# Kernel optimization log

Measured on AMD Instinct MI355X. Metric: run time of the kernel, lower is better.

## Reference

```python
import jax, jax.numpy as jnp
import numpy as np

N = 16384      # total ligand atoms
E = 65536      # edges
B = 256        # graphs / batch
MAXN = 64      # atoms per graph (max_nodes for to_dense_batch)
FIN = 64       # num_node_features
HID = 256      # hidden_channels
GH = 2         # gat heads
LP = 1024      # protein length
NH = 4         # cross-attention heads
HD = HID // NH
VOCAB = 22


def setup_inputs() -> dict:
    key = jax.random.key(0)
    ks = jax.random.split(key, 48)
    f = jnp.float32
    def nrm(k, shape, s=0.05):
        return jax.random.normal(k, shape, f) * s
    inp = {}
    inp["x"] = jax.random.normal(ks[0], (N, FIN), f)
    inp["edge_index"] = jax.random.randint(ks[1], (2, E), 0, N)
    inp["batch"] = jnp.arange(N) // MAXN  # sorted, 64 atoms per graph
    inp["protein_seq"] = jax.random.randint(ks[2], (B, LP), 0, VOCAB)
    # GAT layer 1 (FIN -> HID, GH heads, concat=False)
    inp["w1"] = nrm(ks[3], (FIN, GH * HID)); inp["as1"] = nrm(ks[4], (GH, HID)); inp["ad1"] = nrm(ks[5], (GH, HID)); inp["b1"] = jnp.zeros((HID,), f)
    inp["w2"] = nrm(ks[6], (HID, GH * HID)); inp["as2"] = nrm(ks[7], (GH, HID)); inp["ad2"] = nrm(ks[8], (GH, HID)); inp["b2"] = jnp.zeros((HID,), f)
    inp["w3"] = nrm(ks[9], (HID, GH * HID)); inp["as3"] = nrm(ks[10], (GH, HID)); inp["ad3"] = nrm(ks[11], (GH, HID)); inp["b3"] = jnp.zeros((HID,), f)
    # protein embedding + conv1d (OIH layout)
    inp["emb"] = nrm(ks[12], (VOCAB, HID), 0.1)
    inp["conv_w"] = nrm(ks[13], (HID, HID, 3)); inp["conv_b"] = jnp.zeros((HID,), f)
    # cross-attention MHA
    inp["wq"] = nrm(ks[14], (HID, HID)); inp["bq"] = jnp.zeros((HID,), f)
    inp["wk"] = nrm(ks[15], (HID, HID)); inp["bk"] = jnp.zeros((HID,), f)
    inp["wv"] = nrm(ks[16], (HID, HID)); inp["bv"] = jnp.zeros((HID,), f)
    inp["wo"] = nrm(ks[17], (HID, HID)); inp["bo"] = jnp.zeros((HID,), f)
    inp["ln1_g"] = jnp.ones((HID,), f); inp["ln1_b"] = jnp.zeros((HID,), f)
    inp["ffw1"] = nrm(ks[18], (HID, 4 * HID)); inp["ffb1"] = jnp.zeros((4 * HID,), f)
    inp["ffw2"] = nrm(ks[19], (4 * HID, HID)); inp["ffb2"] = jnp.zeros((HID,), f)
    inp["ln2_g"] = jnp.ones((HID,), f); inp["ln2_b"] = jnp.zeros((HID,), f)
    inp["fc1_w"] = nrm(ks[20], (HID, HID)); inp["fc1_b"] = jnp.zeros((HID,), f)
    inp["fc2_w"] = nrm(ks[21], (HID, 1)); inp["fc2_b"] = jnp.zeros((1,), f)
    return inp


def _gat(x, edge_index, W, a_src, a_dst, bias):
    # PyG GATConv, concat=False (mean over heads), add_self_loops=True
    n = x.shape[0]
    h = (x @ W).reshape(n, GH, HID)                      # [N,GH,C]
    loop = jnp.arange(n)
    src = jnp.concatenate([edge_index[0], loop])
    dst = jnp.concatenate([edge_index[1], loop])
    a_s = jnp.einsum('nhc,hc->nh', h, a_src)             # [N,GH]
    a_d = jnp.einsum('nhc,hc->nh', h, a_dst)
    e = jax.nn.leaky_relu(a_s[src] + a_d[dst], 0.2)      # [E+N,GH]
    emax = jax.ops.segment_max(e, dst, num_segments=n)   # each node has a self-loop
    ex = jnp.exp(e - emax[dst])
    den = jax.ops.segment_sum(ex, dst, num_segments=n)
    alpha = ex / den[dst]                                # [E+N,GH]
    msg = h[src] * alpha[:, :, None]
    out = jax.ops.segment_sum(msg, dst, num_segments=n)  # [N,GH,C]
    return out.mean(axis=1) + bias


def _to_dense_batch(x, batch):
    # batch is sorted node->graph ids; counts per graph <= MAXN
    ones = jnp.ones((x.shape[0],), jnp.int32)
    counts = jax.ops.segment_sum(ones, batch, num_segments=B)
    starts = jnp.cumsum(counts) - counts
    pos = jnp.arange(x.shape[0]) - starts[batch]
    dense = jnp.zeros((B, MAXN, x.shape[1]), x.dtype).at[batch, pos].set(x)
    mask = jnp.zeros((B, MAXN), bool).at[batch, pos].set(True)
    return dense, mask


def _layernorm(x, g, b, eps=1e-5):
    mu = x.mean(-1, keepdims=True)
    var = ((x - mu) ** 2).mean(-1, keepdims=True)
    return (x - mu) * jax.lax.rsqrt(var + eps) * g + b


def reference(x, edge_index, batch, protein_seq,
              w1, as1, ad1, b1, w2, as2, ad2, b2, w3, as3, ad3, b3,
              emb, conv_w, conv_b,
              wq, bq, wk, bk, wv, bv, wo, bo,
              ln1_g, ln1_b, ffw1, ffb1, ffw2, ffb2, ln2_g, ln2_b,
              fc1_w, fc1_b, fc2_w, fc2_b):
    # --- ligand GNN (eval mode: dropout = identity) ---
    h = jax.nn.elu(_gat(x, edge_index, w1, as1, ad1, b1))
    h = jax.nn.elu(_gat(h, edge_index, w2, as2, ad2, b2))
    h = jax.nn.elu(_gat(h, edge_index, w3, as3, ad3, b3))
    lig, lig_mask = _to_dense_batch(h, batch)            # [B,MAXN,HID], [B,MAXN]
    # --- protein branch ---
    p = emb[protein_seq]                                 # [B,LP,HID]
    p = p.transpose(0, 2, 1)                             # [B,HID,LP]
    p = jax.lax.conv_general_dilated(p, conv_w, (1,), [(1, 1)],
                                     dimension_numbers=('NCH', 'OIH', 'NCH'))
    p = jax.nn.relu(p + conv_b[None, :, None]).transpose(0, 2, 1)  # [B,LP,HID]
    kpm = protein_seq == 0                               # key padding mask
    # --- cross attention (query=ligand, key/value=protein) ---
    q = (lig @ wq + bq).reshape(B, MAXN, NH, HD)
    k = (p @ wk + bk).reshape(B, LP, NH, HD)
    v = (p @ wv + bv).reshape(B, LP, NH, HD)
    scores = jnp.einsum('bqhd,bkhd->bhqk', q, k) / np.sqrt(HD).astype(np.float32)
    scores = jnp.where(kpm[:, None, None, :], jnp.float32(-1e9), scores)
    attn = jax.nn.softmax(scores, axis=-1)               # [B,NH,MAXN,LP]
    ctx = jnp.einsum('bhqk,bkhd->bqhd', attn, v).reshape(B, MAXN, HID)
    attn_out = ctx @ wo + bo
    y = _layernorm(lig + attn_out, ln1_g, ln1_b)
    ff = jax.nn.gelu(y @ ffw1 + ffb1, approximate=False) @ ffw2 + ffb2
    y = _layernorm(y + ff, ln2_g, ln2_b)
    # --- masked mean pool ---
    m = lig_mask[:, :, None].astype(y.dtype)
    pooled = (y * m).sum(axis=1) / (m.sum(axis=1) + 1e-6)
    out = jax.nn.relu(pooled @ fc1_w + fc1_b)
    return out @ fc2_w + fc2_b                           # [B,1]
```

## Files before the change

kernel.cpp:

```cpp
#include <hip/hip_runtime.h>
#include <hip/hip_bf16.h>
#include <cstdint>
#include <cstddef>

#define NAT 16384
#define NED 65536
#define BGR 256
#define FIN 64
#define HID 256
#define LPN 1024
#define HD 64
#define NTRIP 11638
#define NTAB  11648

typedef __bf16 bf16x8 __attribute__((ext_vector_type(8)));
typedef float floatx4 __attribute__((ext_vector_type(4)));

__device__ __forceinline__ void gl2lds16(const void* g, void* l)
{
    __builtin_amdgcn_global_load_lds(
        (const __attribute__((address_space(1))) unsigned int*)g,
        (__attribute__((address_space(3))) unsigned int*)l, 16, 0, 0);
}

template<int ACT, int OUTBF16, int BIASROW, int HSPLIT, int NCOL>
__global__ __launch_bounds__(512) void gemm_mfma(const __bf16* __restrict__ A,
    const __bf16* __restrict__ Bt, const float* __restrict__ bias,
    void* __restrict__ Cout, int M, int Nn, int K, float escale)
{
    constexpr int NJ = NCOL / 32;
    __shared__ __bf16 As[2][128][32];
    __shared__ __bf16 Bs[2][NCOL][32];
    const int t = threadIdx.x;
    const int m0 = blockIdx.y * 128, n0 = blockIdx.x * NCOL;
    const int w = t >> 6, lane = t & 63;
    const int wm = (w & 3) * 32, wn = (w >> 2) * (NCOL / 2);
    const int quad = lane >> 4, l16 = lane & 15;
    const int r0 = t >> 2, s0 = t & 3, g0 = (s0 ^ (r0 & 3)) * 8;
    const int fso = (quad ^ (l16 & 3)) * 8;
    floatx4 acc[2][NJ] = {};
    for (int k0 = 0; k0 < K; k0 += 64) {
        gl2lds16(A + (size_t)(m0 + r0) * K + k0 + g0,       &As[0][r0][s0 * 8]);
        gl2lds16(A + (size_t)(m0 + r0) * K + k0 + 32 + g0,  &As[1][r0][s0 * 8]);
        if (NCOL == 128 || t < 256) {
            gl2lds16(Bt + (size_t)(n0 + r0) * K + k0 + g0,      &Bs[0][r0][s0 * 8]);
            gl2lds16(Bt + (size_t)(n0 + r0) * K + k0 + 32 + g0, &Bs[1][r0][s0 * 8]);
        }
        __syncthreads();
#pragma unroll
        for (int c = 0; c < 2; c++) {
            bf16x8 af[2], bfr[NJ];
#pragma unroll
            for (int mi = 0; mi < 2; mi++) af[mi]  = *(const bf16x8*)&As[c][wm + mi * 16 + l16][fso];
#pragma unroll
            for (int nj = 0; nj < NJ; nj++) bfr[nj] = *(const bf16x8*)&Bs[c][wn + nj * 16 + l16][fso];
#pragma unroll
            for (int mi = 0; mi < 2; mi++)
#pragma unroll
                for (int nj = 0; nj < NJ; nj++)
                    acc[mi][nj] = __builtin_amdgcn_mfma_f32_16x16x32_bf16(af[mi], bfr[nj], acc[mi][nj], 0, 0, 0);
        }
        __syncthreads();
    }
#pragma unroll
    for (int mi = 0; mi < 2; mi++)
#pragma unroll
        for (int nj = 0; nj < NJ; nj++) {
            int col = n0 + wn + nj * 16 + l16;
#pragma unroll
            for (int r = 0; r < 4; r++) {
                int row = m0 + wm + mi * 16 + quad * 4 + r;
                float bval = bias ? (BIASROW ? bias[row] : bias[col]) : 0.f;
                float v = (acc[mi][nj][r] + bval) * escale;
                if (ACT == 1) v = fmaxf(v, 0.f);
                if (ACT == 2) v = 0.5f * v * (1.f + erff(v * 0.70710678118654752f));
                if (HSPLIT)      ((__bf16*)Cout)[((size_t)(col >> 6) * M + row) * 64 + (col & 63)] = (__bf16)v;
                else if (OUTBF16) ((__bf16*)Cout)[(size_t)row * Nn + col] = (__bf16)v;
                else              ((float*)Cout)[(size_t)row * Nn + col] = v;
            }
        }
}

__global__ __launch_bounds__(512) void kvtab_k(const __bf16* __restrict__ A,
    const __bf16* __restrict__ wkT, const __bf16* __restrict__ wvT,
    const float* __restrict__ bk, const float* __restrict__ bv,
    __bf16* __restrict__ Ktab, __bf16* __restrict__ Vtab)
{
    __shared__ __bf16 As[2][128][32];
    __shared__ __bf16 Bs[2][128][32];
    const int t = threadIdx.x;
    const int z = blockIdx.x >> 1;
    const int m0 = blockIdx.y * 128, n0 = (blockIdx.x & 1) * 128;
    const __bf16* Bt = z ? wvT : wkT;
    const float* bias = z ? bv : bk;
    __bf16* Cout = z ? Vtab : Ktab;
    const int w = t >> 6, lane = t & 63;
    const int wm = (w & 3) * 32, wn = (w >> 2) * 64;
    const int quad = lane >> 4, l16 = lane & 15;
    const int r0 = t >> 2, s0 = t & 3, g0 = (s0 ^ (r0 & 3)) * 8;
    const int fso = (quad ^ (l16 & 3)) * 8;
    floatx4 acc[2][4] = {};
    for (int k0 = 0; k0 < 256; k0 += 64) {
        gl2lds16(A + (size_t)(m0 + r0) * 256 + k0 + g0,       &As[0][r0][s0 * 8]);
        gl2lds16(A + (size_t)(m0 + r0) * 256 + k0 + 32 + g0,  &As[1][r0][s0 * 8]);
        gl2lds16(Bt + (size_t)(n0 + r0) * 256 + k0 + g0,      &Bs[0][r0][s0 * 8]);
        gl2lds16(Bt + (size_t)(n0 + r0) * 256 + k0 + 32 + g0, &Bs[1][r0][s0 * 8]);
        __syncthreads();
#pragma unroll
        for (int c = 0; c < 2; c++) {
            bf16x8 af[2], bfr[4];
#pragma unroll
            for (int mi = 0; mi < 2; mi++) af[mi]  = *(const bf16x8*)&As[c][wm + mi * 16 + l16][fso];
#pragma unroll
            for (int nj = 0; nj < 4; nj++) bfr[nj] = *(const bf16x8*)&Bs[c][wn + nj * 16 + l16][fso];
#pragma unroll
            for (int mi = 0; mi < 2; mi++)
#pragma unroll
                for (int nj = 0; nj < 4; nj++)
                    acc[mi][nj] = __builtin_amdgcn_mfma_f32_16x16x32_bf16(af[mi], bfr[nj], acc[mi][nj], 0, 0, 0);
        }
        __syncthreads();
    }
#pragma unroll
    for (int mi = 0; mi < 2; mi++)
#pragma unroll
        for (int nj = 0; nj < 4; nj++) {
            int col = n0 + wn + nj * 16 + l16;
#pragma unroll
            for (int r = 0; r < 4; r++) {
                int row = m0 + wm + mi * 16 + quad * 4 + r;
                float v = acc[mi][nj][r] + bias[col];
                Cout[((size_t)(col >> 6) * NTAB + row) * 64 + (col & 63)] = (__bf16)v;
            }
        }
}

__global__ __launch_bounds__(512) void gemm_gat(const __bf16* __restrict__ A,
    const __bf16* __restrict__ Bt, const float* __restrict__ as_f,
    const float* __restrict__ ad_f, __bf16* __restrict__ Hg,
    float* __restrict__ part, int K)
{
    __shared__ __bf16 As[2][128][32];
    __shared__ __bf16 Bs[2][128][32];
    const int t = threadIdx.x;
    const int m0 = blockIdx.y * 128, n0 = blockIdx.x * 128;
    const int w = t >> 6, lane = t & 63;
    const int wm = (w & 3) * 32, wn = (w >> 2) * 64;
    const int quad = lane >> 4, l16 = lane & 15;
    const int r0 = t >> 2, s0 = t & 3, g0 = (s0 ^ (r0 & 3)) * 8;
    const int fso = (quad ^ (l16 & 3)) * 8;
    floatx4 acc[2][4] = {};
    for (int k0 = 0; k0 < K; k0 += 64) {
        gl2lds16(A + (size_t)(m0 + r0) * K + k0 + g0,       &As[0][r0][s0 * 8]);
        gl2lds16(A + (size_t)(m0 + r0) * K + k0 + 32 + g0,  &As[1][r0][s0 * 8]);
        gl2lds16(Bt + (size_t)(n0 + r0) * K + k0 + g0,      &Bs[0][r0][s0 * 8]);
        gl2lds16(Bt + (size_t)(n0 + r0) * K + k0 + 32 + g0, &Bs[1][r0][s0 * 8]);
        __syncthreads();
#pragma unroll
        for (int c = 0; c < 2; c++) {
            bf16x8 af[2], bfr[4];
#pragma unroll
            for (int mi = 0; mi < 2; mi++) af[mi]  = *(const bf16x8*)&As[c][wm + mi * 16 + l16][fso];
#pragma unroll
            for (int nj = 0; nj < 4; nj++) bfr[nj] = *(const bf16x8*)&Bs[c][wn + nj * 16 + l16][fso];
#pragma unroll
            for (int mi = 0; mi < 2; mi++)
#pragma unroll
                for (int nj = 0; nj < 4; nj++)
                    acc[mi][nj] = __builtin_amdgcn_mfma_f32_16x16x32_bf16(af[mi], bfr[nj], acc[mi][nj], 0, 0, 0);
        }
        __syncthreads();
    }
    const int slot = blockIdx.x * 2 + (w >> 2);
#pragma unroll
    for (int mi = 0; mi < 2; mi++) {
#pragma unroll
        for (int r = 0; r < 4; r++) {
            float ps = 0.f, pd = 0.f;
#pragma unroll
            for (int nj = 0; nj < 4; nj++) {
                int col = n0 + wn + nj * 16 + l16;
                float v = acc[mi][nj][r];
                ps += v * as_f[col];
                pd += v * ad_f[col];
            }
#pragma unroll
            for (int off = 1; off < 16; off <<= 1) {
                ps += __shfl_xor(ps, off, 64);
                pd += __shfl_xor(pd, off, 64);
            }
            if (l16 == 0) {
                int row = m0 + wm + mi * 16 + quad * 4 + r;
                part[(size_t)(slot * 2 + 0) * NAT + row] = ps;
                part[(size_t)(slot * 2 + 1) * NAT + row] = pd;
            }
        }
    }
#pragma unroll
    for (int mi = 0; mi < 2; mi++)
#pragma unroll
        for (int nj = 0; nj < 4; nj++) {
            int col = n0 + wn + nj * 16 + l16;
#pragma unroll
            for (int r = 0; r < 4; r++) {
                int row = m0 + wm + mi * 16 + quad * 4 + r;
                Hg[(size_t)row * 512 + col] = (__bf16)acc[mi][nj][r];
            }
        }
}

__global__ void fold_k(const float* __restrict__ part, float* __restrict__ a_s,
                       float* __restrict__ a_d)
{
    int n = blockIdx.x * 256 + threadIdx.x;
    float s0 = 0.f, d0 = 0.f, s1 = 0.f, d1 = 0.f;
#pragma unroll
    for (int sl = 0; sl < 4; sl++) {
        s0 += part[(size_t)(sl * 2 + 0) * NAT + n];
        d0 += part[(size_t)(sl * 2 + 1) * NAT + n];
        s1 += part[(size_t)((sl + 4) * 2 + 0) * NAT + n];
        d1 += part[(size_t)((sl + 4) * 2 + 1) * NAT + n];
    }
    a_s[n * 2 + 0] = s0; a_s[n * 2 + 1] = s1;
    a_d[n * 2 + 0] = d0; a_d[n * 2 + 1] = d1;
}

__global__ __launch_bounds__(256) void tap_k(const float* __restrict__ emb,
    const float* __restrict__ cw, float* __restrict__ tap)
{
    const int dlv = blockIdx.x >> 2, part = blockIdx.x & 3;
    const int dl = dlv / 22, v = dlv % 22;
    const int n = threadIdx.x;
    const float* er = emb + v * 256 + part * 64;
    const float* wr = cw + (size_t)n * 768 + part * 192 + dl;
    float s = 0.f;
    for (int k = 0; k < 64; k += 4) {
        s += er[k + 0] * wr[k * 3 + 0];
        s += er[k + 1] * wr[k * 3 + 3];
        s += er[k + 2] * wr[k * 3 + 6];
        s += er[k + 3] * wr[k * 3 + 9];
    }
    atomicAdd(&tap[(size_t)dlv * 256 + n], s);
}

__global__ __launch_bounds__(256) void ptab_k(const float* __restrict__ tap,
    const float* __restrict__ bias, __bf16* __restrict__ P)
{
    const int t = threadIdx.x;
    const int row = blockIdx.x * 8 + (t >> 5);
    const int c = (t & 31) * 8;
    __bf16 o[8];
    if (row < NTRIP) {
        const int a = row / 506, rem = row - a * 506;
        const int t1 = rem / 23, c2 = rem - t1 * 23;
        float acc[8];
#pragma unroll
        for (int j = 0; j < 8; j++) acc[j] = bias[c + j];
        if (a > 0) {
            const float* r = tap + (size_t)(0 * 22 + (a - 1)) * 256 + c;
#pragma unroll
            for (int j = 0; j < 8; j++) acc[j] += r[j];
        }
        {
            const float* r = tap + (size_t)(1 * 22 + t1) * 256 + c;
#pragma unroll
            for (int j = 0; j < 8; j++) acc[j] += r[j];
        }
        if (c2 > 0) {
            const float* r = tap + (size_t)(2 * 22 + (c2 - 1)) * 256 + c;
#pragma unroll
            for (int j = 0; j < 8; j++) acc[j] += r[j];
        }
#pragma unroll
        for (int j = 0; j < 8; j++) o[j] = (__bf16)fmaxf(acc[j], 0.f);
    } else {
#pragma unroll
        for (int j = 0; j < 8; j++) o[j] = (__bf16)0.f;
    }
    *(uint4*)(P + (size_t)row * 256 + c) = *(uint4*)o;
}

__global__ void tid_k(const int* __restrict__ seq, unsigned short* __restrict__ tid)
{
    int i = blockIdx.x * 256 + threadIdx.x;
    int b = i >> 10, l = i & 1023;
    const int* sr = seq + b * LPN;
    int t0 = (l > 0) ? sr[l - 1] : -1;
    int t1 = sr[l];
    int t2 = (l < LPN - 1) ? sr[l + 1] : -1;
    int v = (t0 + 1) * 506 + t1 * 23 + (t2 + 1);
    tid[i] = (unsigned short)(v | (t1 == 0 ? 0x8000 : 0));
}

struct Segs {
    const float* src[12];
    __bf16* dst[12];
    int kdim[12];
    int ndim[12];
    int mode[12];
    int start[13];
};

__global__ void cvtall_k(Segs S, int total)
{
    int i = blockIdx.x * 256 + threadIdx.x;
    if (i >= total) return;
    int s = 0;
    while (i >= S.start[s + 1]) s++;
    int j = i - S.start[s];
    if (S.mode[s] == 0) {
        S.dst[s][j] = (__bf16)S.src[s][j];
    } else {
        int K = S.kdim[s], N = S.ndim[s];
        int n = j / K, k = j - n * K;
        S.dst[s][j] = (__bf16)S.src[s][(size_t)k * N + n];
    }
}

__global__ void deg_k(const int* __restrict__ ei, int* __restrict__ deg)
{
    int e = blockIdx.x * 256 + threadIdx.x;
    if (e < NED) atomicAdd(&deg[ei[NED + e]], 1);
}

__global__ __launch_bounds__(256) void scan_k(const int* __restrict__ deg, int* __restrict__ rowptr)
{
    __shared__ int part[256];
    int t = threadIdx.x;
    int base = t * 64;
    int s = 0;
#pragma unroll
    for (int i = 0; i < 64; i++) s += deg[base + i];
    part[t] = s;
    __syncthreads();
    for (int off = 1; off < 256; off <<= 1) {
        int v = (t >= off) ? part[t - off] : 0;
        __syncthreads();
        part[t] += v;
        __syncthreads();
    }
    int run = t ? part[t - 1] : 0;
    for (int i = 0; i < 64; i++) { rowptr[base + i] = run; run += deg[base + i]; }
    if (t == 255) rowptr[16384] = run;
}

__global__ void scat_k(const int* __restrict__ ei, int* __restrict__ fill,
                       const int* __restrict__ rowptr, int* __restrict__ csrc,
                       int* __restrict__ cdst)
{
    int e = blockIdx.x * 256 + threadIdx.x;
    if (e >= NED) return;
    int d = ei[NED + e];
    int pos = rowptr[d] + atomicAdd(&fill[d], 1);
    csrc[pos] = ei[e];
    cdst[pos] = d;
}

__global__ void erec_k(const int* __restrict__ csrc, const int* __restrict__ cdst,
    const float* __restrict__ a_s, const float* __restrict__ a_d,
    float4* __restrict__ rec)
{
    int p = blockIdx.x * 256 + threadIdx.x;
    if (p >= NED) return;
    int s = csrc[p], d = cdst[p];
    float2 as2 = *(const float2*)(a_s + s * 2);
    float2 ad2 = *(const float2*)(a_d + d * 2);
    float e0 = as2.x + ad2.x; e0 = (e0 > 0.f) ? e0 : 0.2f * e0;
    float e1 = as2.y + ad2.y; e1 = (e1 > 0.f) ? e1 : 0.2f * e1;
    rec[p] = make_float4(e0, e1, __int_as_float(s), 0.f);
}

__global__ __launch_bounds__(256) void gat_agg(const int* __restrict__ rowptr,
    const float4* __restrict__ rec, const __bf16* __restrict__ hgb,
    const float* __restrict__ a_s, const float* __restrict__ a_d,
    const float* __restrict__ bias, float* __restrict__ out, __bf16* __restrict__ outb)
{
    const int wave = threadIdx.x >> 6, lane = threadIdx.x & 63;
    const int d = blockIdx.x * 4 + wave;
    const int beg = rowptr[d], end = rowptr[d + 1];
    float2 as2 = *(const float2*)(a_s + d * 2);
    float2 ad2 = *(const float2*)(a_d + d * 2);
    float e0 = as2.x + ad2.x; e0 = (e0 > 0.f) ? e0 : 0.2f * e0;
    float e1 = as2.y + ad2.y; e1 = (e1 > 0.f) ? e1 : 0.2f * e1;
    float m0 = e0, den0 = 1.f, m1 = e1, den1 = 1.f;
    for (int p = beg; p < end; p++) {
        float4 rc = rec[p];
        float nm0 = fmaxf(m0, rc.x);
        den0 = den0 * __expf(m0 - nm0) + __expf(rc.x - nm0);
        m0 = nm0;
        float nm1 = fmaxf(m1, rc.y);
        den1 = den1 * __expf(m1 - nm1) + __expf(rc.y - nm1);
        m1 = nm1;
    }
    const float inv0 = 1.f / den0, inv1 = 1.f / den1;
    const int ch = lane * 8;
    const int g = ch >> 8;
    const float mg = g ? m1 : m0, invg = g ? inv1 : inv0;
    float acc[8] = {};
    {
        float al = __expf((g ? e1 : e0) - mg) * invg;
        bf16x8 hv = *(const bf16x8*)(hgb + (size_t)d * 512 + ch);
#pragma unroll
        for (int j = 0; j < 8; j++) acc[j] += (float)hv[j] * al;
    }
    for (int p = beg; p < end; p++) {
        float4 rc = rec[p];
        float al = __expf((g ? rc.y : rc.x) - mg) * invg;
        int s = __float_as_int(rc.z);
        bf16x8 hv = *(const bf16x8*)(hgb + (size_t)s * 512 + ch);
#pragma unroll
        for (int j = 0; j < 8; j++) acc[j] += (float)hv[j] * al;
    }
    float other[8];
#pragma unroll
    for (int j = 0; j < 8; j++) other[j] = __shfl_xor(acc[j], 32, 64);
    if (lane < 32) {
#pragma unroll
        for (int j = 0; j < 8; j++) {
            float v = 0.5f * (acc[j] + other[j]) + bias[ch + j];
            v = (v > 0.f) ? v : expm1f(v);
            if (out) out[(size_t)d * 256 + ch + j] = v;
            outb[(size_t)d * 256 + ch + j] = (__bf16)v;
        }
    }
}

__global__ __launch_bounds__(256, 4) void attn6_k(const __bf16* __restrict__ Qb,
    const __bf16* __restrict__ Ktab, const __bf16* __restrict__ Vtab,
    const unsigned short* __restrict__ tid16, __bf16* __restrict__ O)
{
    __shared__ __bf16 Ks[2][4096];
    __shared__ __bf16 Vs[4096];
    __shared__ __bf16 Ps2[4][16][64];
    __shared__ float mask_f[1024];
    __shared__ unsigned short tids[1024];
    const int t = threadIdx.x;
    const int bid = blockIdx.x;
    const int h = (bid >> 1) & 3;
    const int b = ((bid >> 3) << 1) | (bid & 1);
    const int w = t >> 6, lane = t & 63;
    const int quad = lane >> 4, l16 = lane & 15;
    const int key = (l16 & 7) << 4;
    const __bf16* Kh = Ktab + (size_t)h * NTAB * 64;
    const __bf16* Vh = Vtab + (size_t)h * NTAB * 64;
    {
        const uint32_t* src = (const uint32_t*)(tid16 + (size_t)b * LPN);
        uint32_t v0 = src[t], v1 = src[t + 256];
        ((uint32_t*)tids)[t] = v0;
        ((uint32_t*)tids)[t + 256] = v1;
        mask_f[2 * t + 0] = (v0 & 0x8000u) ? -1e9f : 0.f;
        mask_f[2 * t + 1] = (v0 & 0x80000000u) ? -1e9f : 0.f;
        mask_f[2 * (t + 256) + 0] = (v1 & 0x8000u) ? -1e9f : 0.f;
        mask_f[2 * (t + 256) + 1] = (v1 & 0x80000000u) ? -1e9f : 0.f;
    }
    const __bf16* qrow = Qb + (size_t)(b * 64 + w * 16 + l16) * HID + h * HD;
    bf16x8 aq0 = *(const bf16x8*)(qrow + quad * 8);
    bf16x8 aq1 = *(const bf16x8*)(qrow + 32 + quad * 8);
    __syncthreads();

    auto stageK = [&](int kt, int bufb) {
#pragma unroll
        for (int it = 0; it < 2; it++) {
            const int s = it * 256 + t;
            const int pos = s >> 3;
            const int c = (s & 7) ^ (pos & 7);
            const int row = tids[kt * 64 + pos] & 0x7fff;
            gl2lds16(Kh + (size_t)row * 64 + c * 8,
                     &Ks[bufb][(it * 256 + w * 64) * 8]);
        }
    };
    auto loadV = [&](int kt, bf16x8* vrr) {
#pragma unroll
        for (int it = 0; it < 2; it++) {
            const int pos = w * 8 + (lane >> 3) + it * 32;
            const int row = tids[kt * 64 + pos] & 0x7fff;
            vrr[it] = *(const bf16x8*)(Vh + (size_t)row * 64 + (lane & 7) * 8);
        }
    };
    auto writeV = [&](const bf16x8* vrr) {
        const int p = lane >> 3, c = lane & 7;
#pragma unroll
        for (int it = 0; it < 2; it++) {
            const int pos = w * 8 + p + it * 32;
            const int cp = pos >> 3;
#pragma unroll
            for (int j = 0; j < 8; j++) {
                const int chl = c * 8 + j;
                Vs[chl * 64 + (((cp ^ c ^ j) & 7) << 3) + p] = vrr[it][j];
            }
        }
    };

    bf16x8 vr[2];
    stageK(0, 0);
    loadV(0, vr);
    writeV(vr);
    float m_run = -3e38f;
    float l_run = 0.f;
    floatx4 ctx[4] = {};
    __syncthreads();

    for (int kt = 0; kt < 16; kt++) {
        const int buf = kt & 1;
        const int kp0 = kt * 64;
        if (kt < 15) {
            stageK(kt + 1, buf ^ 1);
            loadV(kt + 1, vr);
        }
        const int ksl0 = (quad ^ (l16 & 7)) * 8;
        const int ksl1 = ((quad + 4) ^ (l16 & 7)) * 8;
        floatx4 s[4];
#pragma unroll
        for (int nj = 0; nj < 4; nj++) {
            const __bf16* kr = &Ks[buf][(nj * 16 + l16) * 64];
            bf16x8 k0 = *(const bf16x8*)&kr[ksl0];
            bf16x8 k1 = *(const bf16x8*)&kr[ksl1];
            floatx4 z = {0.f, 0.f, 0.f, 0.f};
            s[nj] = __builtin_amdgcn_mfma_f32_16x16x32_bf16(k0, aq0, z, 0, 0, 0);
            s[nj] = __builtin_amdgcn_mfma_f32_16x16x32_bf16(k1, aq1, s[nj], 0, 0, 0);
        }
#pragma unroll
        for (int nj = 0; nj < 4; nj++) {
            floatx4 m4 = *(const floatx4*)&mask_f[kp0 + nj * 16 + quad * 4];
#pragma unroll
            for (int r = 0; r < 4; r++) s[nj][r] += m4[r];
        }
        float mx = -3e38f;
#pragma unroll
        for (int nj = 0; nj < 4; nj++)
#pragma unroll
            for (int r = 0; r < 4; r++) mx = fmaxf(mx, s[nj][r]);
        mx = fmaxf(mx, __shfl_xor(mx, 16, 64));
        mx = fmaxf(mx, __shfl_xor(mx, 32, 64));
        const float mn = fmaxf(m_run, mx);
        const float alpha = __expf(m_run - mn);
        m_run = mn;
        float rs = 0.f;
#pragma unroll
        for (int nj = 0; nj < 4; nj++)
#pragma unroll
            for (int r = 0; r < 4; r++) {
                float p = __expf(s[nj][r] - mn);
                s[nj][r] = p;
                rs += p;
            }
        rs += __shfl_xor(rs, 16, 64);
        rs += __shfl_xor(rs, 32, 64);
        l_run = l_run * alpha + rs;
        float al[4];
#pragma unroll
        for (int r = 0; r < 4; r++) al[r] = __shfl(alpha, quad * 4 + r, 64);
        {
            char* rowp = (char*)&Ps2[w][l16][0];
#pragma unroll
            for (int nj = 0; nj < 4; nj++) {
                union { uint2 u2; unsigned short us[4]; } pk;
#pragma unroll
                for (int r = 0; r < 4; r++) {
                    __bf16 bv = (__bf16)s[nj][r];
                    pk.us[r] = *(unsigned short*)&bv;
                }
                *(uint2*)(rowp + ((nj * 32 + quad * 8) ^ key)) = pk.u2;
            }
        }
        bf16x8 pa0 = *(const bf16x8*)((char*)&Ps2[w][l16][0] + ((quad * 16) ^ key));
        bf16x8 pa1 = *(const bf16x8*)((char*)&Ps2[w][l16][0] + ((64 + quad * 16) ^ key));
#pragma unroll
        for (int dj = 0; dj < 4; dj++) {
#pragma unroll
            for (int r = 0; r < 4; r++) ctx[dj][r] *= al[r];
            const int chl = dj * 16 + l16;
            const int Xc = ((chl >> 3) ^ (chl & 7)) & 7;
            bf16x8 bv0 = *(const bf16x8*)&Vs[chl * 64 + (((quad ^ Xc) & 7) << 3)];
            bf16x8 bv1 = *(const bf16x8*)&Vs[chl * 64 + ((((quad + 4) ^ Xc) & 7) << 3)];
            ctx[dj] = __builtin_amdgcn_mfma_f32_16x16x32_bf16(pa0, bv0, ctx[dj], 0, 0, 0);
            ctx[dj] = __builtin_amdgcn_mfma_f32_16x16x32_bf16(pa1, bv1, ctx[dj], 0, 0, 0);
        }
        __syncthreads();
        if (kt < 15) writeV(vr);
        __syncthreads();
    }
    float ll[4];
#pragma unroll
    for (int r = 0; r < 4; r++) ll[r] = __shfl(l_run, quad * 4 + r, 64);
#pragma unroll
    for (int dj = 0; dj < 4; dj++)
#pragma unroll
        for (int r = 0; r < 4; r++) {
            int q = w * 16 + quad * 4 + r;
            O[((size_t)(b * 64 + q)) * 256 + h * HD + dj * 16 + l16] = (__bf16)(ctx[dj][r] / ll[r]);
        }
}

__device__ __forceinline__ float blockSum256(float v, float* red)
{
#pragma unroll
    for (int off = 32; off >= 1; off >>= 1) v += __shfl_down(v, off, 64);
    int wave = threadIdx.x >> 6, lane = threadIdx.x & 63;
    if (lane == 0) red[wave] = v;
    __syncthreads();
    float s = red[0] + red[1] + red[2] + red[3];
    __syncthreads();
    return s;
}

__global__ __launch_bounds__(256) void lnres_k(const float* __restrict__ A,
    const float* __restrict__ Bb, const float* __restrict__ g,
    const float* __restrict__ be, float* __restrict__ Y, __bf16* __restrict__ Yb)
{
    __shared__ float red[4];
    int r = blockIdx.x, t = threadIdx.x;
    float v = A[(size_t)r * 256 + t] + Bb[(size_t)r * 256 + t];
    float mean = blockSum256(v, red) * (1.f / 256.f);
    float d = v - mean;
    float var = blockSum256(d * d, red) * (1.f / 256.f);
    float o = d * rsqrtf(var + 1e-5f) * g[t] + be[t];
    Y[(size_t)r * 256 + t] = o;
    if (Yb) Yb[(size_t)r * 256 + t] = (__bf16)o;
}

__global__ __launch_bounds__(256) void head_k(const float* __restrict__ Y,
    const float* __restrict__ fc1w, const float* __restrict__ fc1b,
    const float* __restrict__ fc2w, const float* __restrict__ fc2b,
    float* __restrict__ out)
{
    __shared__ float pooled[256];
    __shared__ float h[256];
    __shared__ float red[4];
    int b = blockIdx.x, t = threadIdx.x;
    float s = 0.f;
#pragma unroll 8
    for (int q = 0; q < 64; q++) s += Y[(size_t)(b * 64 + q) * 256 + t];
    pooled[t] = s / (64.f + 1e-6f);
    __syncthreads();
    float a = 0.f;
    for (int k = 0; k < 256; k += 4) {
        a += pooled[k + 0] * fc1w[(k + 0) * 256 + t];
        a += pooled[k + 1] * fc1w[(k + 1) * 256 + t];
        a += pooled[k + 2] * fc1w[(k + 2) * 256 + t];
        a += pooled[k + 3] * fc1w[(k + 3) * 256 + t];
    }
    h[t] = fmaxf(a + fc1b[t], 0.f);
    __syncthreads();
    float p = h[t] * fc2w[t];
    p = blockSum256(p, red);
    if (t == 0) out[b] = p + fc2b[0];
}

extern "C" void kernel_launch(void* const* d_in, const int* in_sizes, int n_in,
                              void* d_out, int out_size, void* d_ws, size_t ws_size,
                              hipStream_t stream)
{
    const float* x     = (const float*)d_in[0];
    const int*   ei    = (const int*)d_in[1];
    const int*   pseq  = (const int*)d_in[3];
    const float* w1  = (const float*)d_in[4];
    const float* as1 = (const float*)d_in[5];
    const float* ad1 = (const float*)d_in[6];
    const float* b1  = (const float*)d_in[7];
    const float* w2  = (const float*)d_in[8];
    const float* as2 = (const float*)d_in[9];
    const float* ad2 = (const float*)d_in[10];
    const float* b2  = (const float*)d_in[11];
    const float* w3  = (const float*)d_in[12];
    const float* as3 = (const float*)d_in[13];
    const float* ad3 = (const float*)d_in[14];
    const float* b3  = (const float*)d_in[15];
    const float* emb    = (const float*)d_in[16];
    const float* conv_w = (const float*)d_in[17];
    const float* conv_b = (const float*)d_in[18];
    const float* wq = (const float*)d_in[19];
    const float* bq = (const float*)d_in[20];
    const float* wk = (const float*)d_in[21];
    const float* bk = (const float*)d_in[22];
    const float* wv = (const float*)d_in[23];
    const float* bv = (const float*)d_in[24];
    const float* wo = (const float*)d_in[25];
    const float* bo = (const float*)d_in[26];
    const float* ln1_g = (const float*)d_in[27];
    const float* ln1_b = (const float*)d_in[28];
    const float* ffw1  = (const float*)d_in[29];
    const float* ffb1  = (const float*)d_in[30];
    const float* ffw2  = (const float*)d_in[31];
    const float* ffb2  = (const float*)d_in[32];
    const float* ln2_g = (const float*)d_in[33];
    const float* ln2_b = (const float*)d_in[34];
    const float* fc1_w = (const float*)d_in[35];
    const float* fc1_b = (const float*)d_in[36];
    const float* fc2_w = (const float*)d_in[37];
    const float* fc2_b = (const float*)d_in[38];
    (void)in_sizes; (void)n_in; (void)out_size;

    char* ws = (char*)d_ws;
    size_t off = 0;
    auto alloc = [&](size_t bytes) -> char* {
        char* p = ws + off;
        off += (bytes + 255) & ~(size_t)255;
        return p;
    };
    __bf16* hgb  = (__bf16*)alloc((size_t)NAT * 512 * 2);
    float* og    = (float*)alloc((size_t)NAT * 512 * 4);
    float* hb0   = (float*)alloc((size_t)NAT * 256 * 4);
    float* hb1   = (float*)alloc((size_t)NAT * 256 * 4);
    __bf16* xb   = (__bf16*)alloc((size_t)NAT * FIN * 2);
    __bf16* hbb  = (__bf16*)alloc((size_t)NAT * 256 * 2);
    __bf16* qbb  = (__bf16*)alloc((size_t)NAT * 256 * 2);
    __bf16* ctxbb= (__bf16*)alloc((size_t)NAT * 256 * 2);
    __bf16* ybb  = (__bf16*)alloc((size_t)NAT * 256 * 2);
    float* a_s   = (float*)alloc((size_t)NAT * 2 * 4);
    float* a_d   = (float*)alloc((size_t)NAT * 2 * 4);
    float* asd_p = (float*)alloc((size_t)16 * NAT * 4);
    int* deg     = (int*)alloc((size_t)NAT * 4);
    int* fill    = (int*)alloc((size_t)NAT * 4);
    int* rowptr  = (int*)alloc((size_t)(NAT + 1) * 4);
    int* csrc    = (int*)alloc((size_t)NED * 4);
    int* cdst    = (int*)alloc((size_t)NED * 4);
    float4* erec = (float4*)alloc((size_t)NED * 16);
    float* tap   = (float*)alloc((size_t)3 * 22 * 256 * 4);
    __bf16* ptab = (__bf16*)alloc((size_t)NTAB * 256 * 2);
    __bf16* Ktab = (__bf16*)alloc((size_t)NTAB * 256 * 2);
    __bf16* Vtab = (__bf16*)alloc((size_t)NTAB * 256 * 2);
    unsigned short* tid16 = (unsigned short*)alloc((size_t)BGR * LPN * 2);
    __bf16* w1T  = (__bf16*)alloc((size_t)512 * 64 * 2);
    __bf16* w2T  = (__bf16*)alloc((size_t)512 * 256 * 2);
    __bf16* w3T  = (__bf16*)alloc((size_t)512 * 256 * 2);
    __bf16* wkT  = (__bf16*)alloc((size_t)256 * 256 * 2);
    __bf16* wvT  = (__bf16*)alloc((size_t)256 * 256 * 2);
    __bf16* wqT  = (__bf16*)alloc((size_t)256 * 256 * 2);
    __bf16* woT  = (__bf16*)alloc((size_t)256 * 256 * 2);
    __bf16* f1T  = (__bf16*)alloc((size_t)1024 * 256 * 2);
    __bf16* f2T  = (__bf16*)alloc((size_t)256 * 1024 * 2);
    size_t fixed_end = off;
    char* region   = ws + fixed_end;
    __bf16* ffbb   = (__bf16*)region;
    float*  y2     = (float*)(region + (size_t)NAT * 1024 * 2);
    float* attno = og;
    float* ybuf  = og + (size_t)NAT * 256;
    float* ff2o  = hb1;
    (void)ws_size;

    hipMemsetAsync(deg, 0, (size_t)NAT * 8, stream);
    hipMemsetAsync(tap, 0, (size_t)3 * 22 * 256 * 4, stream);
    deg_k<<<NED / 256, 256, 0, stream>>>(ei, deg);
    scan_k<<<1, 256, 0, stream>>>(deg, rowptr);
    scat_k<<<NED / 256, 256, 0, stream>>>(ei, fill, rowptr, csrc, cdst);
    tap_k<<<264, 256, 0, stream>>>(emb, conv_w, tap);

    {
        Segs S;
        const float* srcs[10] = {x, w1, w2, w3, wk, wv, wq, wo, ffw1, ffw2};
        __bf16* dsts[10] = {xb, w1T, w2T, w3T, wkT, wvT, wqT, woT, f1T, f2T};
        int kd[10] = {0, 64, 256, 256, 256, 256, 256, 256, 256, 1024};
        int nd[10] = {0, 512, 512, 512, 256, 256, 256, 256, 1024, 256};
        int md[10] = {0, 1, 1, 1, 1, 1, 1, 1, 1, 1};
        int cnt[10] = {NAT * FIN, 32768, 131072, 131072,
                       65536, 65536, 65536, 65536, 262144, 262144};
        int run = 0;
        for (int i = 0; i < 10; i++) {
            S.src[i] = srcs[i]; S.dst[i] = dsts[i];
            S.kdim[i] = kd[i]; S.ndim[i] = nd[i]; S.mode[i] = md[i];
            S.start[i] = run; run += cnt[i];
        }
        S.start[10] = run; S.start[11] = run; S.start[12] = run;
        cvtall_k<<<(run + 255) / 256, 256, 0, stream>>>(S, run);
    }

    ptab_k<<<NTAB / 8, 256, 0, stream>>>(tap, conv_b, ptab);
    tid_k<<<BGR * LPN / 256, 256, 0, stream>>>(pseq, tid16);
    kvtab_k<<<dim3(4, NTAB / 128), 512, 0, stream>>>(ptab, wkT, wvT, bk, bv, Ktab, Vtab);

    const __bf16* WT[3] = {w1T, w2T, w3T};
    const float* asl[3] = {as1, as2, as3};
    const float* adl[3] = {ad1, ad2, ad3};
    const float* bl[3]  = {b1, b2, b3};
    float* houts[3] = {nullptr, nullptr, hb0};
    const __bf16* hinb = xb;
    int Kdim = FIN;
    for (int l = 0; l < 3; l++) {
        gemm_gat<<<dim3(4, NAT / 128), 512, 0, stream>>>(hinb, WT[l], asl[l], adl[l], hgb, asd_p, Kdim);
        fold_k<<<NAT / 256, 256, 0, stream>>>(asd_p, a_s, a_d);
        erec_k<<<NED / 256, 256, 0, stream>>>(csrc, cdst, a_s, a_d, erec);
        gat_agg<<<NAT / 4, 256, 0, stream>>>(rowptr, erec, hgb, a_s, a_d, bl[l], houts[l], hbb);
        hinb = hbb;
        Kdim = HID;
    }
    const float* lig = hb0;
    const __bf16* ligb = hbb;

    gemm_mfma<0, 1, 0, 0, 64><<<dim3(4, NAT / 128), 512, 0, stream>>>(ligb, wqT, bq, qbb, NAT, 256, 256, 0.125f);

    attn6_k<<<BGR * 4, 256, 0, stream>>>(qbb, Ktab, Vtab, tid16, ctxbb);

    gemm_mfma<0, 0, 0, 0, 64><<<dim3(4, NAT / 128), 512, 0, stream>>>(ctxbb, woT, bo, attno, NAT, 256, 256, 1.f);
    lnres_k<<<NAT, 256, 0, stream>>>(lig, attno, ln1_g, ln1_b, ybuf, ybb);
    gemm_mfma<2, 1, 0, 0, 128><<<dim3(8, NAT / 128), 512, 0, stream>>>(ybb, f1T, ffb1, ffbb, NAT, 1024, 256, 1.f);
    gemm_mfma<0, 0, 0, 0, 64><<<dim3(4, NAT / 128), 512, 0, stream>>>(ffbb, f2T, ffb2, ff2o, NAT, 256, 1024, 1.f);
    lnres_k<<<NAT, 256, 0, stream>>>(ybuf, ff2o, ln2_g, ln2_b, y2, nullptr);

    head_k<<<BGR, 256, 0, stream>>>(y2, fc1_w, fc1_b, fc2_w, fc2_b, (float*)d_out);
}
```

Measured before the change: 492.5 us.

## Merge setup kernels into three launches and drop per-layer edge-record pass

Independent preprocessing kernels (degree count, conv tap table, token ids, weight conversion, scan, protein table, CSR scatter, K/V table GEMM) are grouped by dependency level into three multi-role kernels, cutting about seven launches. The per-layer erec_k pass that precomputed edge logits is removed. gat_agg now recomputes the leaky-relu logits from csrc and a_s inline in both of its loops, trading extra gathers and math for one fewer kernel and buffer per layer. Mixing heterogeneous block roles in one grid may leave some blocks idle or unbalanced.

Measured after the change: 475.0 us. 1.04x faster.

```diff
diff --git a/kernel.cpp b/kernel.cpp
--- a/kernel.cpp
+++ b/kernel.cpp
@@ -81,60 +81,6 @@
         }
 }
 
-__global__ __launch_bounds__(512) void kvtab_k(const __bf16* __restrict__ A,
-    const __bf16* __restrict__ wkT, const __bf16* __restrict__ wvT,
-    const float* __restrict__ bk, const float* __restrict__ bv,
-    __bf16* __restrict__ Ktab, __bf16* __restrict__ Vtab)
-{
-    __shared__ __bf16 As[2][128][32];
-    __shared__ __bf16 Bs[2][128][32];
-    const int t = threadIdx.x;
-    const int z = blockIdx.x >> 1;
-    const int m0 = blockIdx.y * 128, n0 = (blockIdx.x & 1) * 128;
-    const __bf16* Bt = z ? wvT : wkT;
-    const float* bias = z ? bv : bk;
-    __bf16* Cout = z ? Vtab : Ktab;
-    const int w = t >> 6, lane = t & 63;
-    const int wm = (w & 3) * 32, wn = (w >> 2) * 64;
-    const int quad = lane >> 4, l16 = lane & 15;
-    const int r0 = t >> 2, s0 = t & 3, g0 = (s0 ^ (r0 & 3)) * 8;
-    const int fso = (quad ^ (l16 & 3)) * 8;
-    floatx4 acc[2][4] = {};
-    for (int k0 = 0; k0 < 256; k0 += 64) {
-        gl2lds16(A + (size_t)(m0 + r0) * 256 + k0 + g0,       &As[0][r0][s0 * 8]);
-        gl2lds16(A + (size_t)(m0 + r0) * 256 + k0 + 32 + g0,  &As[1][r0][s0 * 8]);
-        gl2lds16(Bt + (size_t)(n0 + r0) * 256 + k0 + g0,      &Bs[0][r0][s0 * 8]);
-        gl2lds16(Bt + (size_t)(n0 + r0) * 256 + k0 + 32 + g0, &Bs[1][r0][s0 * 8]);
-        __syncthreads();
-#pragma unroll
-        for (int c = 0; c < 2; c++) {
-            bf16x8 af[2], bfr[4];
-#pragma unroll
-            for (int mi = 0; mi < 2; mi++) af[mi]  = *(const bf16x8*)&As[c][wm + mi * 16 + l16][fso];
-#pragma unroll
-            for (int nj = 0; nj < 4; nj++) bfr[nj] = *(const bf16x8*)&Bs[c][wn + nj * 16 + l16][fso];
-#pragma unroll
-            for (int mi = 0; mi < 2; mi++)
-#pragma unroll
-                for (int nj = 0; nj < 4; nj++)
-                    acc[mi][nj] = __builtin_amdgcn_mfma_f32_16x16x32_bf16(af[mi], bfr[nj], acc[mi][nj], 0, 0, 0);
-        }
-        __syncthreads();
-    }
-#pragma unroll
-    for (int mi = 0; mi < 2; mi++)
-#pragma unroll
-        for (int nj = 0; nj < 4; nj++) {
-            int col = n0 + wn + nj * 16 + l16;
-#pragma unroll
-            for (int r = 0; r < 4; r++) {
-                int row = m0 + wm + mi * 16 + quad * 4 + r;
-                float v = acc[mi][nj][r] + bias[col];
-                Cout[((size_t)(col >> 6) * NTAB + row) * 64 + (col & 63)] = (__bf16)v;
-            }
-        }
-}
-
 __global__ __launch_bounds__(512) void gemm_gat(const __bf16* __restrict__ A,
     const __bf16* __restrict__ Bt, const float* __restrict__ as_f,
     const float* __restrict__ ad_f, __bf16* __restrict__ Hg,
@@ -225,73 +171,6 @@
     a_d[n * 2 + 0] = d0; a_d[n * 2 + 1] = d1;
 }
 
-__global__ __launch_bounds__(256) void tap_k(const float* __restrict__ emb,
-    const float* __restrict__ cw, float* __restrict__ tap)
-{
-    const int dlv = blockIdx.x >> 2, part = blockIdx.x & 3;
-    const int dl = dlv / 22, v = dlv % 22;
-    const int n = threadIdx.x;
-    const float* er = emb + v * 256 + part * 64;
-    const float* wr = cw + (size_t)n * 768 + part * 192 + dl;
-    float s = 0.f;
-    for (int k = 0; k < 64; k += 4) {
-        s += er[k + 0] * wr[k * 3 + 0];
-        s += er[k + 1] * wr[k * 3 + 3];
-        s += er[k + 2] * wr[k * 3 + 6];
-        s += er[k + 3] * wr[k * 3 + 9];
-    }
-    atomicAdd(&tap[(size_t)dlv * 256 + n], s);
-}
-
-__global__ __launch_bounds__(256) void ptab_k(const float* __restrict__ tap,
-    const float* __restrict__ bias, __bf16* __restrict__ P)
-{
-    const int t = threadIdx.x;
-    const int row = blockIdx.x * 8 + (t >> 5);
-    const int c = (t & 31) * 8;
-    __bf16 o[8];
-    if (row < NTRIP) {
-        const int a = row / 506, rem = row - a * 506;
-        const int t1 = rem / 23, c2 = rem - t1 * 23;
-        float acc[8];
-#pragma unroll
-        for (int j = 0; j < 8; j++) acc[j] = bias[c + j];
-        if (a > 0) {
-            const float* r = tap + (size_t)(0 * 22 + (a - 1)) * 256 + c;
-#pragma unroll
-            for (int j = 0; j < 8; j++) acc[j] += r[j];
-        }
-        {
-            const float* r = tap + (size_t)(1 * 22 + t1) * 256 + c;
-#pragma unroll
-            for (int j = 0; j < 8; j++) acc[j] += r[j];
-        }
-        if (c2 > 0) {
-            const float* r = tap + (size_t)(2 * 22 + (c2 - 1)) * 256 + c;
-#pragma unroll
-            for (int j = 0; j < 8; j++) acc[j] += r[j];
-        }
-#pragma unroll
-        for (int j = 0; j < 8; j++) o[j] = (__bf16)fmaxf(acc[j], 0.f);
-    } else {
-#pragma unroll
-        for (int j = 0; j < 8; j++) o[j] = (__bf16)0.f;
-    }
-    *(uint4*)(P + (size_t)row * 256 + c) = *(uint4*)o;
-}
-
-__global__ void tid_k(const int* __restrict__ seq, unsigned short* __restrict__ tid)
-{
-    int i = blockIdx.x * 256 + threadIdx.x;
-    int b = i >> 10, l = i & 1023;
-    const int* sr = seq + b * LPN;
-    int t0 = (l > 0) ? sr[l - 1] : -1;
-    int t1 = sr[l];
-    int t2 = (l < LPN - 1) ? sr[l + 1] : -1;
-    int v = (t0 + 1) * 506 + t1 * 23 + (t2 + 1);
-    tid[i] = (unsigned short)(v | (t1 == 0 ? 0x8000 : 0));
-}
-
 struct Segs {
     const float* src[12];
     __bf16* dst[12];
@@ -301,77 +180,183 @@
     int start[13];
 };
 
-__global__ void cvtall_k(Segs S, int total)
-{
-    int i = blockIdx.x * 256 + threadIdx.x;
-    if (i >= total) return;
-    int s = 0;
-    while (i >= S.start[s + 1]) s++;
-    int j = i - S.start[s];
-    if (S.mode[s] == 0) {
-        S.dst[s][j] = (__bf16)S.src[s][j];
+__global__ __launch_bounds__(256) void misc1_k(const int* __restrict__ ei,
+    int* __restrict__ deg, const float* __restrict__ emb,
+    const float* __restrict__ cw, float* __restrict__ tap,
+    const int* __restrict__ seq, unsigned short* __restrict__ tid,
+    Segs S, int total)
+{
+    const int bid = blockIdx.x;
+    const int t = threadIdx.x;
+    if (bid < 256) {
+        int e = bid * 256 + t;
+        atomicAdd(&deg[ei[NED + e]], 1);
+    } else if (bid < 520) {
+        const int b = bid - 256;
+        const int dlv = b >> 2, part = b & 3;
+        const int dl = dlv / 22, v = dlv % 22;
+        const float* er = emb + v * 256 + part * 64;
+        const float* wr = cw + (size_t)t * 768 + part * 192 + dl;
+        float s = 0.f;
+        for (int k = 0; k < 64; k += 4) {
+            s += er[k + 0] * wr[k * 3 + 0];
+            s += er[k + 1] * wr[k * 3 + 3];
+            s += er[k + 2] * wr[k * 3 + 6];
+            s += er[k + 3] * wr[k * 3 + 9];
+        }
+        atomicAdd(&tap[(size_t)dlv * 256 + t], s);
+    } else if (bid < 1544) {
+        int i = (bid - 520) * 256 + t;
+        int b = i >> 10, l = i & 1023;
+        const int* sr = seq + b * LPN;
+        int t0 = (l > 0) ? sr[l - 1] : -1;
+        int t1 = sr[l];
+        int t2 = (l < LPN - 1) ? sr[l + 1] : -1;
+        int v = (t0 + 1) * 506 + t1 * 23 + (t2 + 1);
+        tid[i] = (unsigned short)(v | (t1 == 0 ? 0x8000 : 0));
     } else {
-        int K = S.kdim[s], N = S.ndim[s];
-        int n = j / K, k = j - n * K;
-        S.dst[s][j] = (__bf16)S.src[s][(size_t)k * N + n];
-    }
-}
-
-__global__ void deg_k(const int* __restrict__ ei, int* __restrict__ deg)
-{
-    int e = blockIdx.x * 256 + threadIdx.x;
-    if (e < NED) atomicAdd(&deg[ei[NED + e]], 1);
-}
-
-__global__ __launch_bounds__(256) void scan_k(const int* __restrict__ deg, int* __restrict__ rowptr)
+        int i = (bid - 1544) * 256 + t;
+        if (i >= total) return;
+        int s = 0;
+        while (i >= S.start[s + 1]) s++;
+        int j = i - S.start[s];
+        if (S.mode[s] == 0) {
+            S.dst[s][j] = (__bf16)S.src[s][j];
+        } else {
+            int K = S.kdim[s], N = S.ndim[s];
+            int n = j / K, k = j - n * K;
+            S.dst[s][j] = (__bf16)S.src[s][(size_t)k * N + n];
+        }
+    }
+}
+
+__global__ __launch_bounds__(256) void misc2_k(const int* __restrict__ deg,
+    int* __restrict__ rowptr, const float* __restrict__ tap,
+    const float* __restrict__ bias, __bf16* __restrict__ P)
 {
     __shared__ int part[256];
-    int t = threadIdx.x;
-    int base = t * 64;
-    int s = 0;
-#pragma unroll
-    for (int i = 0; i < 64; i++) s += deg[base + i];
-    part[t] = s;
-    __syncthreads();
-    for (int off = 1; off < 256; off <<= 1) {
-        int v = (t >= off) ? part[t - off] : 0;
-        __syncthreads();
-        part[t] += v;
-        __syncthreads();
-    }
-    int run = t ? part[t - 1] : 0;
-    for (int i = 0; i < 64; i++) { rowptr[base + i] = run; run += deg[base + i]; }
-    if (t == 255) rowptr[16384] = run;
-}
-
-__global__ void scat_k(const int* __restrict__ ei, int* __restrict__ fill,
-                       const int* __restrict__ rowptr, int* __restrict__ csrc,
-                       int* __restrict__ cdst)
-{
-    int e = blockIdx.x * 256 + threadIdx.x;
-    if (e >= NED) return;
-    int d = ei[NED + e];
-    int pos = rowptr[d] + atomicAdd(&fill[d], 1);
-    csrc[pos] = ei[e];
-    cdst[pos] = d;
-}
-
-__global__ void erec_k(const int* __restrict__ csrc, const int* __restrict__ cdst,
-    const float* __restrict__ a_s, const float* __restrict__ a_d,
-    float4* __restrict__ rec)
-{
-    int p = blockIdx.x * 256 + threadIdx.x;
-    if (p >= NED) return;
-    int s = csrc[p], d = cdst[p];
-    float2 as2 = *(const float2*)(a_s + s * 2);
-    float2 ad2 = *(const float2*)(a_d + d * 2);
-    float e0 = as2.x + ad2.x; e0 = (e0 > 0.f) ? e0 : 0.2f * e0;
-    float e1 = as2.y + ad2.y; e1 = (e1 > 0.f) ? e1 : 0.2f * e1;
-    rec[p] = make_float4(e0, e1, __int_as_float(s), 0.f);
+    const int t = threadIdx.x;
+    if (blockIdx.x == 0) {
+        int base = t * 64;
+        int s = 0;
+#pragma unroll
+        for (int i = 0; i < 64; i++) s += deg[base + i];
+        part[t] = s;
+        __syncthreads();
+        for (int off = 1; off < 256; off <<= 1) {
+            int v = (t >= off) ? part[t - off] : 0;
+            __syncthreads();
+            part[t] += v;
+            __syncthreads();
+        }
+        int run = t ? part[t - 1] : 0;
+        for (int i = 0; i < 64; i++) { rowptr[base + i] = run; run += deg[base + i]; }
+        if (t == 255) rowptr[16384] = run;
+    } else {
+        const int row = (blockIdx.x - 1) * 8 + (t >> 5);
+        const int c = (t & 31) * 8;
+        __bf16 o[8];
+        if (row < NTRIP) {
+            const int a = row / 506, rem = row - a * 506;
+            const int t1 = rem / 23, c2 = rem - t1 * 23;
+            float acc[8];
+#pragma unroll
+            for (int j = 0; j < 8; j++) acc[j] = bias[c + j];
+            if (a > 0) {
+                const float* r = tap + (size_t)(0 * 22 + (a - 1)) * 256 + c;
+#pragma unroll
+                for (int j = 0; j < 8; j++) acc[j] += r[j];
+            }
+            {
+                const float* r = tap + (size_t)(1 * 22 + t1) * 256 + c;
+#pragma unroll
+                for (int j = 0; j < 8; j++) acc[j] += r[j];
+            }
+            if (c2 > 0) {
+                const float* r = tap + (size_t)(2 * 22 + (c2 - 1)) * 256 + c;
+#pragma unroll
+                for (int j = 0; j < 8; j++) acc[j] += r[j];
+            }
+#pragma unroll
+            for (int j = 0; j < 8; j++) o[j] = (__bf16)fmaxf(acc[j], 0.f);
+        } else {
+#pragma unroll
+            for (int j = 0; j < 8; j++) o[j] = (__bf16)0.f;
+        }
+        *(uint4*)(P + (size_t)row * 256 + c) = *(uint4*)o;
+    }
+}
+
+__global__ __launch_bounds__(512) void misc3_k(const int* __restrict__ ei,
+    int* __restrict__ fill, const int* __restrict__ rowptr,
+    int* __restrict__ csrc, int* __restrict__ cdst,
+    const __bf16* __restrict__ A, const __bf16* __restrict__ wkT,
+    const __bf16* __restrict__ wvT, const float* __restrict__ bk,
+    const float* __restrict__ bv, __bf16* __restrict__ Ktab,
+    __bf16* __restrict__ Vtab)
+{
+    __shared__ __bf16 As[2][128][32];
+    __shared__ __bf16 Bs[2][128][32];
+    const int t = threadIdx.x;
+    if (blockIdx.x < 128) {
+        int e = blockIdx.x * 512 + t;
+        if (e >= NED) return;
+        int d = ei[NED + e];
+        int pos = rowptr[d] + atomicAdd(&fill[d], 1);
+        csrc[pos] = ei[e];
+        cdst[pos] = d;
+        return;
+    }
+    const int lb = blockIdx.x - 128;
+    const int bx = lb & 3, by = lb >> 2;
+    const int z = bx >> 1;
+    const int m0 = by * 128, n0 = (bx & 1) * 128;
+    const __bf16* Bt = z ? wvT : wkT;
+    const float* bias = z ? bv : bk;
+    __bf16* Cout = z ? Vtab : Ktab;
+    const int w = t >> 6, lane = t & 63;
+    const int wm = (w & 3) * 32, wn = (w >> 2) * 64;
+    const int quad = lane >> 4, l16 = lane & 15;
+    const int r0 = t >> 2, s0 = t & 3, g0 = (s0 ^ (r0 & 3)) * 8;
+    const int fso = (quad ^ (l16 & 3)) * 8;
+    floatx4 acc[2][4] = {};
+    for (int k0 = 0; k0 < 256; k0 += 64) {
+        gl2lds16(A + (size_t)(m0 + r0) * 256 + k0 + g0,       &As[0][r0][s0 * 8]);
+        gl2lds16(A + (size_t)(m0 + r0) * 256 + k0 + 32 + g0,  &As[1][r0][s0 * 8]);
+        gl2lds16(Bt + (size_t)(n0 + r0) * 256 + k0 + g0,      &Bs[0][r0][s0 * 8]);
+        gl2lds16(Bt + (size_t)(n0 + r0) * 256 + k0 + 32 + g0, &Bs[1][r0][s0 * 8]);
+        __syncthreads();
+#pragma unroll
+        for (int c = 0; c < 2; c++) {
+            bf16x8 af[2], bfr[4];
+#pragma unroll
+            for (int mi = 0; mi < 2; mi++) af[mi]  = *(const bf16x8*)&As[c][wm + mi * 16 + l16][fso];
+#pragma unroll
+            for (int nj = 0; nj < 4; nj++) bfr[nj] = *(const bf16x8*)&Bs[c][wn + nj * 16 + l16][fso];
+#pragma unroll
+            for (int mi = 0; mi < 2; mi++)
+#pragma unroll
+                for (int nj = 0; nj < 4; nj++)
+                    acc[mi][nj] = __builtin_amdgcn_mfma_f32_16x16x32_bf16(af[mi], bfr[nj], acc[mi][nj], 0, 0, 0);
+        }
+        __syncthreads();
+    }
+#pragma unroll
+    for (int mi = 0; mi < 2; mi++)
+#pragma unroll
+        for (int nj = 0; nj < 4; nj++) {
+            int col = n0 + wn + nj * 16 + l16;
+#pragma unroll
+            for (int r = 0; r < 4; r++) {
+                int row = m0 + wm + mi * 16 + quad * 4 + r;
+                float v = acc[mi][nj][r] + bias[col];
+                Cout[((size_t)(col >> 6) * NTAB + row) * 64 + (col & 63)] = (__bf16)v;
+            }
+        }
 }
 
 __global__ __launch_bounds__(256) void gat_agg(const int* __restrict__ rowptr,
-    const float4* __restrict__ rec, const __bf16* __restrict__ hgb,
+    const int* __restrict__ csrc, const __bf16* __restrict__ hgb,
     const float* __restrict__ a_s, const float* __restrict__ a_d,
     const float* __restrict__ bias, float* __restrict__ out, __bf16* __restrict__ outb)
 {
@@ -384,12 +369,15 @@
     float e1 = as2.y + ad2.y; e1 = (e1 > 0.f) ? e1 : 0.2f * e1;
     float m0 = e0, den0 = 1.f, m1 = e1, den1 = 1.f;
     for (int p = beg; p < end; p++) {
-        float4 rc = rec[p];
-        float nm0 = fmaxf(m0, rc.x);
-        den0 = den0 * __expf(m0 - nm0) + __expf(rc.x - nm0);
+        int s = csrc[p];
+        float2 av = *(const float2*)(a_s + s * 2);
+        float f0 = av.x + ad2.x; f0 = (f0 > 0.f) ? f0 : 0.2f * f0;
+        float f1 = av.y + ad2.y; f1 = (f1 > 0.f) ? f1 : 0.2f * f1;
+        float nm0 = fmaxf(m0, f0);
+        den0 = den0 * __expf(m0 - nm0) + __expf(f0 - nm0);
         m0 = nm0;
-        float nm1 = fmaxf(m1, rc.y);
-        den1 = den1 * __expf(m1 - nm1) + __expf(rc.y - nm1);
+        float nm1 = fmaxf(m1, f1);
+        den1 = den1 * __expf(m1 - nm1) + __expf(f1 - nm1);
         m1 = nm1;
     }
     const float inv0 = 1.f / den0, inv1 = 1.f / den1;
@@ -404,9 +392,11 @@
         for (int j = 0; j < 8; j++) acc[j] += (float)hv[j] * al;
     }
     for (int p = beg; p < end; p++) {
-        float4 rc = rec[p];
-        float al = __expf((g ? rc.y : rc.x) - mg) * invg;
-        int s = __float_as_int(rc.z);
+        int s = csrc[p];
+        float2 av = *(const float2*)(a_s + s * 2);
+        float f0 = av.x + ad2.x; f0 = (f0 > 0.f) ? f0 : 0.2f * f0;
+        float f1 = av.y + ad2.y; f1 = (f1 > 0.f) ? f1 : 0.2f * f1;
+        float al = __expf((g ? f1 : f0) - mg) * invg;
         bf16x8 hv = *(const bf16x8*)(hgb + (size_t)s * 512 + ch);
 #pragma unroll
         for (int j = 0; j < 8; j++) acc[j] += (float)hv[j] * al;
@@ -715,7 +705,6 @@
     int* rowptr  = (int*)alloc((size_t)(NAT + 1) * 4);
     int* csrc    = (int*)alloc((size_t)NED * 4);
     int* cdst    = (int*)alloc((size_t)NED * 4);
-    float4* erec = (float4*)alloc((size_t)NED * 16);
     float* tap   = (float*)alloc((size_t)3 * 22 * 256 * 4);
     __bf16* ptab = (__bf16*)alloc((size_t)NTAB * 256 * 2);
     __bf16* Ktab = (__bf16*)alloc((size_t)NTAB * 256 * 2);
@@ -741,11 +730,8 @@
 
     hipMemsetAsync(deg, 0, (size_t)NAT * 8, stream);
     hipMemsetAsync(tap, 0, (size_t)3 * 22 * 256 * 4, stream);
-    deg_k<<<NED / 256, 256, 0, stream>>>(ei, deg);
-    scan_k<<<1, 256, 0, stream>>>(deg, rowptr);
-    scat_k<<<NED / 256, 256, 0, stream>>>(ei, fill, rowptr, csrc, cdst);
-    tap_k<<<264, 256, 0, stream>>>(emb, conv_w, tap);
-
+
+    int cvt_total;
     {
         Segs S;
         const float* srcs[10] = {x, w1, w2, w3, wk, wv, wq, wo, ffw1, ffw2};
@@ -762,12 +748,15 @@
             S.start[i] = run; run += cnt[i];
         }
         S.start[10] = run; S.start[11] = run; S.start[12] = run;
-        cvtall_k<<<(run + 255) / 256, 256, 0, stream>>>(S, run);
-    }
-
-    ptab_k<<<NTAB / 8, 256, 0, stream>>>(tap, conv_b, ptab);
-    tid_k<<<BGR * LPN / 256, 256, 0, stream>>>(pseq, tid16);
-    kvtab_k<<<dim3(4, NTAB / 128), 512, 0, stream>>>(ptab, wkT, wvT, bk, bv, Ktab, Vtab);
+        cvt_total = run;
+        int grid1 = 1544 + (run + 255) / 256;
+        misc1_k<<<grid1, 256, 0, stream>>>(ei, deg, emb, conv_w, tap, pseq, tid16, S, run);
+    }
+
+    misc2_k<<<1 + NTAB / 8, 256, 0, stream>>>(deg, rowptr, tap, conv_b, ptab);
+
+    misc3_k<<<128 + 4 * (NTAB / 128), 512, 0, stream>>>(ei, fill, rowptr, csrc, cdst,
+                                                        ptab, wkT, wvT, bk, bv, Ktab, Vtab);
 
     const __bf16* WT[3] = {w1T, w2T, w3T};
     const float* asl[3] = {as1, as2, as3};
@@ -779,8 +768,7 @@
     for (int l = 0; l < 3; l++) {
         gemm_gat<<<dim3(4, NAT / 128), 512, 0, stream>>>(hinb, WT[l], asl[l], adl[l], hgb, asd_p, Kdim);
         fold_k<<<NAT / 256, 256, 0, stream>>>(asd_p, a_s, a_d);
-        erec_k<<<NED / 256, 256, 0, stream>>>(csrc, cdst, a_s, a_d, erec);
-        gat_agg<<<NAT / 4, 256, 0, stream>>>(rowptr, erec, hgb, a_s, a_d, bl[l], houts[l], hbb);
+        gat_agg<<<NAT / 4, 256, 0, stream>>>(rowptr, csrc, hgb, a_s, a_d, bl[l], houts[l], hbb);
         hinb = hbb;
         Kdim = HID;
     }
```
